# Kernel optimization log

Hardware: AMD Instinct MI355X
Metric: run time of the kernel (lower is better)

## Reference

```python
import jax, jax.numpy as jnp
import numpy as np
import math

B, H, N, D = 2, 8, 2048, 64

def setup_inputs() -> dict:
    key = jax.random.key(0)
    k1, k2, k3, k4, k5 = jax.random.split(key, 5)
    query = jax.random.normal(k1, (B, H, N, D), dtype=jnp.float32)
    k = jax.random.normal(k2, (B, H, N, D), dtype=jnp.float32)
    value = jax.random.normal(k3, (B, H, N, D), dtype=jnp.float32)
    mask = jax.random.randint(k4, (B, H, N, N), 0, 2, dtype=jnp.int32)
    p = jax.random.uniform(k5, (B, H, N, N), dtype=jnp.float32)
    return {"query": query, "key": k, "value": value, "mask": mask, "p": p}

def reference(query, key, value, mask, p):
    # scores: [B,H,N,N] = QK^T / sqrt(d)
    scores = jnp.einsum('bhqd,bhkd->bhqk', query, key) / math.sqrt(query.shape[-1])
    # additive log-probability bias
    scores = scores + jnp.log(p + 1e-12)
    # mask==0 -> -1e9
    scores = jnp.where(mask == 0, jnp.float32(-1e9), scores)
    p_attn = jax.nn.softmax(scores, axis=-1)
    out = jnp.einsum('bhqk,bhkd->bhqd', p_attn, value)
    return (out, p_attn)
```

## Files before the change

kernel.cpp:

```cpp
#include <hip/hip_runtime.h>


typedef float  f4v   __attribute__((ext_vector_type(4)));
typedef int    i4v   __attribute__((ext_vector_type(4)));
typedef __bf16 bf16x8 __attribute__((ext_vector_type(8)));
typedef unsigned short us8 __attribute__((ext_vector_type(8)));
typedef unsigned short us4 __attribute__((ext_vector_type(4)));
typedef unsigned int   u4v __attribute__((ext_vector_type(4)));

#define MFMA16(a,b,c) __builtin_amdgcn_mfma_f32_16x16x32_bf16((a),(b),(c),0,0,0)

static __device__ __forceinline__ unsigned short f2bf(float f){
  unsigned u = __builtin_bit_cast(unsigned, f);
  u += 0x7fffu + ((u >> 16) & 1u);
  return (unsigned short)(u >> 16);
}
static __device__ __forceinline__ bf16x8 ldg8(const unsigned short* p){
  u4v v = *(const u4v*)p;
  return __builtin_bit_cast(bf16x8, v);
}

__global__ void prep_qk(const float* __restrict__ Q, const float* __restrict__ K,
                        unsigned short* __restrict__ Qb, unsigned short* __restrict__ Kb){
  int i = blockIdx.x * 256 + threadIdx.x;
  int base = i * 4;
  f4v q = *(const f4v*)(Q + base);
  f4v k = *(const f4v*)(K + base);
  us4 qo, ko;
#pragma unroll
  for(int j=0;j<4;j++){ qo[j] = f2bf(q[j] * 0.125f); ko[j] = f2bf(k[j]); }
  *(us4*)(Qb + base) = qo;
  *(us4*)(Kb + base) = ko;
}

__global__ void prep_vt(const float* __restrict__ V, unsigned short* __restrict__ Vt){
  int t   = blockIdx.x * 256 + threadIdx.x;
  int bh  = t >> 14;
  int rem = t & 16383;
  int d   = rem >> 8;
  int n0  = (rem & 255) * 8;
  const float* src = V + (((long)bh*2048 + n0) * 64 + d);
  us8 o;
#pragma unroll
  for(int j=0;j<8;j++) o[j] = f2bf(src[j*64]);
  *(us8*)(Vt + ((long)(bh*64 + d)) * 2048 + n0) = o;
}

__global__ __launch_bounds__(256, 2) void attn_main(
    const float* __restrict__ P, const int* __restrict__ M,
    const unsigned short* __restrict__ Qb, const unsigned short* __restrict__ Kb,
    const unsigned short* __restrict__ Vt,
    float* __restrict__ out_o, float* __restrict__ out_p){

  __shared__ float stage[4*2*528];
  __shared__ float wred[2][4][16];
  __shared__ float obuf[4][16][64];

  const int tid  = threadIdx.x;
  const int w    = tid >> 6;
  const int lane = tid & 63;
  const int m    = lane & 15;
  const int q    = lane >> 4;
  const int bidx = blockIdx.x;
  const int bh = ((bidx & 7) << 1) | ((bidx >> 3) & 1);
  const int qt = bidx >> 4;
  const int q0 = qt << 4;
  const int wbase = w << 9;

  const long  rowQ  = (long)bh*2048 + q0 + m;
  const long  pbase = rowQ * 2048;
  const unsigned short* Qrow = Qb + rowQ * 64;
  const bf16x8 qf0 = ldg8(Qrow + q*8);
  const bf16x8 qf1 = ldg8(Qrow + 32 + q*8);
  const unsigned short* Kbh = Kb + ((long)bh << 17);
  const unsigned short* Vbh = Vt + ((long)bh << 17);

  float sreg[16][8];
  float vmax = -3.0e38f;
  float* st0 = stage + w * 1056;

#pragma unroll
  for(int c=0;c<16;c++){
    float* st = st0 + (c & 1) * 528;
    const int k0 = wbase + c*32;
    const unsigned short* Kp = Kbh + (long)(k0 + m)*64 + q*8;
    bf16x8 kf00 = ldg8(Kp);
    bf16x8 kf01 = ldg8(Kp + 32);
    bf16x8 kf10 = ldg8(Kp + 16*64);
    bf16x8 kf11 = ldg8(Kp + 16*64 + 32);
    const float* pp = P + pbase + k0 + q*8;
    f4v pv0 = *(const f4v*)pp;
    f4v pv1 = *(const f4v*)(pp + 4);
    const int* mp = M + pbase + k0 + q*8;
    i4v mv0 = *(const i4v*)mp;
    i4v mv1 = *(const i4v*)(mp + 4);

    f4v acc0 = {0.f,0.f,0.f,0.f}, acc1 = {0.f,0.f,0.f,0.f};
    acc0 = MFMA16(qf0, kf00, acc0);
    acc0 = MFMA16(qf1, kf01, acc0);
    acc1 = MFMA16(qf0, kf10, acc1);
    acc1 = MFMA16(qf1, kf11, acc1);

#pragma unroll
    for(int r=0;r<4;r++){
      st[(4*q + r)*33 + m]      = acc0[r];
      st[(4*q + r)*33 + 16 + m] = acc1[r];
    }
    float sv[8];
#pragma unroll
    for(int j=0;j<8;j++) sv[j] = st[m*33 + q*8 + j];

#pragma unroll
    for(int j=0;j<8;j++){
      float pj = (j < 4) ? pv0[j] : pv1[j-4];
      int   mj = (j < 4) ? mv0[j] : mv1[j-4];
      float s  = sv[j] + __logf(pj + 1e-12f);
      s = (mj == 0) ? -1.0e9f : s;
      sreg[c][j] = s;
      vmax = fmaxf(vmax, s);
    }
  }

  vmax = fmaxf(vmax, __shfl_xor(vmax, 16));
  vmax = fmaxf(vmax, __shfl_xor(vmax, 32));
  if(lane < 16) wred[0][w][lane] = vmax;
  __syncthreads();
  const float mrow = fmaxf(fmaxf(wred[0][0][m], wred[0][1][m]),
                           fmaxf(wred[0][2][m], wred[0][3][m]));

  float vsum = 0.f;
#pragma unroll
  for(int c=0;c<16;c++){
#pragma unroll
    for(int j=0;j<8;j++){
      float e = __expf(sreg[c][j] - mrow);
      sreg[c][j] = e;
      vsum += e;
    }
  }
  vsum += __shfl_xor(vsum, 16);
  vsum += __shfl_xor(vsum, 32);
  if(lane < 16) wred[1][w][lane] = vsum;
  __syncthreads();
  const float lsum = wred[1][0][m] + wred[1][1][m] + wred[1][2][m] + wred[1][3][m];
  const float rl = 1.0f / lsum;

  f4v o0={0.f,0.f,0.f,0.f}, o1={0.f,0.f,0.f,0.f}, o2={0.f,0.f,0.f,0.f}, o3={0.f,0.f,0.f,0.f};
#pragma unroll
  for(int c=0;c<16;c++){
    const int k0 = wbase + c*32;
    f4v w0, w1; us8 pb;
#pragma unroll
    for(int j=0;j<8;j++){
      float pr = sreg[c][j] * rl;
      if(j < 4) w0[j] = pr; else w1[j-4] = pr;
      pb[j] = f2bf(pr);
    }
    float* op = out_p + pbase + k0 + q*8;
    *(f4v*)op       = w0;
    *(f4v*)(op + 4) = w1;
    bf16x8 af = __builtin_bit_cast(bf16x8, pb);
    const unsigned short* Vp = Vbh + (long)m*2048 + k0 + q*8;
    o0 = MFMA16(af, ldg8(Vp),           o0);
    o1 = MFMA16(af, ldg8(Vp + 16*2048), o1);
    o2 = MFMA16(af, ldg8(Vp + 32*2048), o2);
    o3 = MFMA16(af, ldg8(Vp + 48*2048), o3);
  }

#pragma unroll
  for(int r=0;r<4;r++){
    obuf[w][4*q + r][m]      = o0[r];
    obuf[w][4*q + r][16 + m] = o1[r];
    obuf[w][4*q + r][32 + m] = o2[r];
    obuf[w][4*q + r][48 + m] = o3[r];
  }
  __syncthreads();
  const int row = tid >> 4, cg = (tid & 15) << 2;
  f4v a0 = *(const f4v*)&obuf[0][row][cg];
  f4v a1 = *(const f4v*)&obuf[1][row][cg];
  f4v a2 = *(const f4v*)&obuf[2][row][cg];
  f4v a3 = *(const f4v*)&obuf[3][row][cg];
  f4v s = a0 + a1 + a2 + a3;
  *(f4v*)(out_o + ((long)bh*2048 + q0 + row)*64 + cg) = s;
}

extern "C" void kernel_launch(void* const* d_in, const int* in_sizes, int n_in,
                              void* d_out, int out_size, void* d_ws, size_t ws_size,
                              hipStream_t stream){
  const float* Q = (const float*)d_in[0];
  const float* K = (const float*)d_in[1];
  const float* V = (const float*)d_in[2];
  const int*   M = (const int*)  d_in[3];
  const float* P = (const float*)d_in[4];

  float* out_o = (float*)d_out;
  float* out_p = out_o + (size_t)2*8*2048*64;

  unsigned short* Qb = (unsigned short*)d_ws;
  unsigned short* Kb = Qb + (size_t)2*8*2048*64;
  unsigned short* Vt = Kb + (size_t)2*8*2048*64;

  prep_qk<<<2048, 256, 0, stream>>>(Q, K, Qb, Kb);
  prep_vt<<<1024, 256, 0, stream>>>(V, Vt);
  attn_main<<<2048, 256, 0, stream>>>(P, M, Qb, Kb, Vt, out_o, out_p);
}
```

Baseline: 747.9 us.

## Use 8 waves per block with online softmax and fp16 score storage

The main kernel now runs 512 threads per block, so each wave covers 256 keys instead of 512. Softmax becomes an online running max and sum per chunk, and exponentials are kept in packed fp16 registers that are rescaled at write-out. The next chunk's K, P and mask loads are software-prefetched to overlap with the current chunk's compute, and the V transpose goes through an LDS tile so global accesses are coalesced. The goal is lower register pressure and more waves in flight for this memory-bound kernel, at the cost of fp16 rounding on the stored probabilities and extra exp work.

```diff
diff --git a/kernel.cpp b/kernel.cpp
--- a/kernel.cpp
+++ b/kernel.cpp
@@ -2,11 +2,13 @@
 
 
 typedef float  f4v   __attribute__((ext_vector_type(4)));
+typedef float  f2v   __attribute__((ext_vector_type(2)));
 typedef int    i4v   __attribute__((ext_vector_type(4)));
 typedef __bf16 bf16x8 __attribute__((ext_vector_type(8)));
 typedef unsigned short us8 __attribute__((ext_vector_type(8)));
 typedef unsigned short us4 __attribute__((ext_vector_type(4)));
 typedef unsigned int   u4v __attribute__((ext_vector_type(4)));
+typedef __fp16 h2v  __attribute__((ext_vector_type(2)));
 
 #define MFMA16(a,b,c) __builtin_amdgcn_mfma_f32_16x16x32_bf16((a),(b),(c),0,0,0)
 
@@ -14,6 +16,9 @@
   unsigned u = __builtin_bit_cast(unsigned, f);
   u += 0x7fffu + ((u >> 16) & 1u);
   return (unsigned short)(u >> 16);
+}
+static __device__ __forceinline__ bf16x8 bc8(u4v v){
+  return __builtin_bit_cast(bf16x8, v);
 }
 static __device__ __forceinline__ bf16x8 ldg8(const unsigned short* p){
   u4v v = *(const u4v*)p;
@@ -34,27 +39,44 @@
 }
 
 __global__ void prep_vt(const float* __restrict__ V, unsigned short* __restrict__ Vt){
-  int t   = blockIdx.x * 256 + threadIdx.x;
-  int bh  = t >> 14;
-  int rem = t & 16383;
-  int d   = rem >> 8;
-  int n0  = (rem & 255) * 8;
-  const float* src = V + (((long)bh*2048 + n0) * 64 + d);
-  us8 o;
-#pragma unroll
-  for(int j=0;j<8;j++) o[j] = f2bf(src[j*64]);
-  *(us8*)(Vt + ((long)(bh*64 + d)) * 2048 + n0) = o;
-}
-
-__global__ __launch_bounds__(256, 2) void attn_main(
-    const float* __restrict__ P, const int* __restrict__ M,
+  __shared__ float tile[64*65];
+  const int bh = blockIdx.x >> 5;
+  const int n0 = (blockIdx.x & 31) << 6;
+  const int t  = threadIdx.x;
+  {
+    const int r  = t >> 2;
+    const int c0 = (t & 3) << 4;
+    const float* src = V + ((long)bh*2048 + n0 + r)*64 + c0;
+    f4v v0 = *(const f4v*)(src);
+    f4v v1 = *(const f4v*)(src + 4);
+    f4v v2 = *(const f4v*)(src + 8);
+    f4v v3 = *(const f4v*)(src + 12);
+    float* d = tile + r*65 + c0;
+#pragma unroll
+    for(int j=0;j<4;j++){ d[j]=v0[j]; d[4+j]=v1[j]; d[8+j]=v2[j]; d[12+j]=v3[j]; }
+  }
+  __syncthreads();
+  const int d  = t >> 2;
+  const int g0 = (t & 3) << 1;
+#pragma unroll
+  for(int gi=0; gi<2; gi++){
+    const int g = g0 + gi;
+    us8 o;
+#pragma unroll
+    for(int j=0;j<8;j++) o[j] = f2bf(tile[(g*8 + j)*65 + d]);
+    *(us8*)(Vt + ((long)bh*64 + d)*2048 + n0 + g*8) = o;
+  }
+}
+
+__global__ __launch_bounds__(512, 4) void attn_main(
+    const float* __restrict__ P, const int* __restrict__ Mk,
     const unsigned short* __restrict__ Qb, const unsigned short* __restrict__ Kb,
     const unsigned short* __restrict__ Vt,
     float* __restrict__ out_o, float* __restrict__ out_p){
 
-  __shared__ float stage[4*2*528];
-  __shared__ float wred[2][4][16];
-  __shared__ float obuf[4][16][64];
+  __shared__ float smem[8*1056];
+  __shared__ float wredm[8][16];
+  __shared__ float wreds[8][16];
 
   const int tid  = threadIdx.x;
   const int w    = tid >> 6;
@@ -65,7 +87,7 @@
   const int bh = ((bidx & 7) << 1) | ((bidx >> 3) & 1);
   const int qt = bidx >> 4;
   const int q0 = qt << 4;
-  const int wbase = w << 9;
+  const int wbase = w << 8;
 
   const long  rowQ  = (long)bh*2048 + q0 + m;
   const long  pbase = rowQ * 2048;
@@ -75,86 +97,109 @@
   const unsigned short* Kbh = Kb + ((long)bh << 17);
   const unsigned short* Vbh = Vt + ((long)bh << 17);
 
-  float sreg[16][8];
-  float vmax = -3.0e38f;
-  float* st0 = stage + w * 1056;
-
-#pragma unroll
-  for(int c=0;c<16;c++){
-    float* st = st0 + (c & 1) * 528;
-    const int k0 = wbase + c*32;
-    const unsigned short* Kp = Kbh + (long)(k0 + m)*64 + q*8;
-    bf16x8 kf00 = ldg8(Kp);
-    bf16x8 kf01 = ldg8(Kp + 32);
-    bf16x8 kf10 = ldg8(Kp + 16*64);
-    bf16x8 kf11 = ldg8(Kp + 16*64 + 32);
-    const float* pp = P + pbase + k0 + q*8;
-    f4v pv0 = *(const f4v*)pp;
-    f4v pv1 = *(const f4v*)(pp + 4);
-    const int* mp = M + pbase + k0 + q*8;
-    i4v mv0 = *(const i4v*)mp;
-    i4v mv1 = *(const i4v*)(mp + 4);
-
+  const unsigned short* Kp = Kbh + (long)(wbase + m)*64 + q*8;
+  const float* pp = P  + pbase + wbase + q*8;
+  const int*   mp = Mk + pbase + wbase + q*8;
+
+  h2v   ereg[8][4];
+  float mch[8];
+  float mcur = -3.0e38f, vsum = 0.f;
+  float* st0 = smem + w*1056;
+
+  u4v k0A = *(const u4v*)(Kp);
+  u4v k1A = *(const u4v*)(Kp + 32);
+  u4v k2A = *(const u4v*)(Kp + 1024);
+  u4v k3A = *(const u4v*)(Kp + 1024 + 32);
+  f4v p0A = *(const f4v*)(pp);
+  f4v p1A = *(const f4v*)(pp + 4);
+  i4v m0A = *(const i4v*)(mp);
+  i4v m1A = *(const i4v*)(mp + 4);
+
+#pragma unroll
+  for(int c=0;c<8;c++){
+    u4v k0N,k1N,k2N,k3N; f4v p0N,p1N; i4v m0N,m1N;
+    if(c < 7){
+      const unsigned short* Kn = Kp + (c+1)*2048;
+      k0N = *(const u4v*)(Kn);
+      k1N = *(const u4v*)(Kn + 32);
+      k2N = *(const u4v*)(Kn + 1024);
+      k3N = *(const u4v*)(Kn + 1024 + 32);
+      p0N = *(const f4v*)(pp + (c+1)*32);
+      p1N = *(const f4v*)(pp + (c+1)*32 + 4);
+      m0N = *(const i4v*)(mp + (c+1)*32);
+      m1N = *(const i4v*)(mp + (c+1)*32 + 4);
+    }
     f4v acc0 = {0.f,0.f,0.f,0.f}, acc1 = {0.f,0.f,0.f,0.f};
-    acc0 = MFMA16(qf0, kf00, acc0);
-    acc0 = MFMA16(qf1, kf01, acc0);
-    acc1 = MFMA16(qf0, kf10, acc1);
-    acc1 = MFMA16(qf1, kf11, acc1);
-
+    acc0 = MFMA16(qf0, bc8(k0A), acc0);
+    acc0 = MFMA16(qf1, bc8(k1A), acc0);
+    acc1 = MFMA16(qf0, bc8(k2A), acc1);
+    acc1 = MFMA16(qf1, bc8(k3A), acc1);
+
+    float* st = st0 + (c & 1)*528;
 #pragma unroll
     for(int r=0;r<4;r++){
       st[(4*q + r)*33 + m]      = acc0[r];
       st[(4*q + r)*33 + 16 + m] = acc1[r];
     }
-    float sv[8];
-#pragma unroll
-    for(int j=0;j<8;j++) sv[j] = st[m*33 + q*8 + j];
-
+    float s[8];
 #pragma unroll
     for(int j=0;j<8;j++){
-      float pj = (j < 4) ? pv0[j] : pv1[j-4];
-      int   mj = (j < 4) ? mv0[j] : mv1[j-4];
-      float s  = sv[j] + __logf(pj + 1e-12f);
-      s = (mj == 0) ? -1.0e9f : s;
-      sreg[c][j] = s;
-      vmax = fmaxf(vmax, s);
-    }
-  }
-
-  vmax = fmaxf(vmax, __shfl_xor(vmax, 16));
-  vmax = fmaxf(vmax, __shfl_xor(vmax, 32));
-  if(lane < 16) wred[0][w][lane] = vmax;
+      float pj = (j < 4) ? p0A[j] : p1A[j-4];
+      int   mj = (j < 4) ? m0A[j] : m1A[j-4];
+      float sc = st[m*33 + q*8 + j] + __logf(pj + 1e-12f);
+      s[j] = (mj == 0) ? -1.0e9f : sc;
+    }
+    float cm = s[0];
+#pragma unroll
+    for(int j=1;j<8;j++) cm = fmaxf(cm, s[j]);
+    float mn = fmaxf(mcur, cm);
+    vsum *= __expf(mcur - mn);
+#pragma unroll
+    for(int jj=0;jj<4;jj++){
+      float e0 = __expf(s[2*jj]   - mn);
+      float e1 = __expf(s[2*jj+1] - mn);
+      vsum += e0 + e1;
+      ereg[c][jj] = __builtin_amdgcn_cvt_pkrtz(e0, e1);
+    }
+    mch[c] = mn; mcur = mn;
+
+    k0A=k0N; k1A=k1N; k2A=k2N; k3A=k3N;
+    p0A=p0N; p1A=p1N; m0A=m0N; m1A=m1N;
+  }
+
+  {
+    float om = __shfl_xor(mcur, 16), ov = __shfl_xor(vsum, 16);
+    float nm = fmaxf(mcur, om);
+    vsum = vsum*__expf(mcur - nm) + ov*__expf(om - nm); mcur = nm;
+    om = __shfl_xor(mcur, 32); ov = __shfl_xor(vsum, 32);
+    nm = fmaxf(mcur, om);
+    vsum = vsum*__expf(mcur - nm) + ov*__expf(om - nm); mcur = nm;
+  }
+  if(lane < 16){ wredm[w][lane] = mcur; wreds[w][lane] = vsum; }
   __syncthreads();
-  const float mrow = fmaxf(fmaxf(wred[0][0][m], wred[0][1][m]),
-                           fmaxf(wred[0][2][m], wred[0][3][m]));
-
-  float vsum = 0.f;
-#pragma unroll
-  for(int c=0;c<16;c++){
-#pragma unroll
-    for(int j=0;j<8;j++){
-      float e = __expf(sreg[c][j] - mrow);
-      sreg[c][j] = e;
-      vsum += e;
-    }
-  }
-  vsum += __shfl_xor(vsum, 16);
-  vsum += __shfl_xor(vsum, 32);
-  if(lane < 16) wred[1][w][lane] = vsum;
-  __syncthreads();
-  const float lsum = wred[1][0][m] + wred[1][1][m] + wred[1][2][m] + wred[1][3][m];
-  const float rl = 1.0f / lsum;
+  float Mrow = -3.0e38f;
+#pragma unroll
+  for(int p2=0;p2<8;p2++) Mrow = fmaxf(Mrow, wredm[p2][m]);
+  float l = 0.f;
+#pragma unroll
+  for(int p2=0;p2<8;p2++) l += wreds[p2][m]*__expf(wredm[p2][m] - Mrow);
+  const float rl = 1.0f / l;
 
   f4v o0={0.f,0.f,0.f,0.f}, o1={0.f,0.f,0.f,0.f}, o2={0.f,0.f,0.f,0.f}, o3={0.f,0.f,0.f,0.f};
 #pragma unroll
-  for(int c=0;c<16;c++){
+  for(int c=0;c<8;c++){
+    const float f = __expf(mch[c] - Mrow) * rl;
     const int k0 = wbase + c*32;
     f4v w0, w1; us8 pb;
 #pragma unroll
-    for(int j=0;j<8;j++){
-      float pr = sreg[c][j] * rl;
-      if(j < 4) w0[j] = pr; else w1[j-4] = pr;
-      pb[j] = f2bf(pr);
+    for(int jj=0;jj<4;jj++){
+      h2v ee = ereg[c][jj];
+      float pr0 = (float)ee[0] * f;
+      float pr1 = (float)ee[1] * f;
+      if(jj < 2){ w0[2*jj] = pr0; w0[2*jj+1] = pr1; }
+      else      { w1[2*jj-4] = pr0; w1[2*jj-3] = pr1; }
+      pb[2*jj]   = f2bf(pr0);
+      pb[2*jj+1] = f2bf(pr1);
     }
     float* op = out_p + pbase + k0 + q*8;
     *(f4v*)op       = w0;
@@ -167,21 +212,24 @@
     o3 = MFMA16(af, ldg8(Vp + 48*2048), o3);
   }
 
+  float* ob = smem + w*1056;
 #pragma unroll
   for(int r=0;r<4;r++){
-    obuf[w][4*q + r][m]      = o0[r];
-    obuf[w][4*q + r][16 + m] = o1[r];
-    obuf[w][4*q + r][32 + m] = o2[r];
-    obuf[w][4*q + r][48 + m] = o3[r];
+    ob[(4*q + r)*66 + m]      = o0[r];
+    ob[(4*q + r)*66 + 16 + m] = o1[r];
+    ob[(4*q + r)*66 + 32 + m] = o2[r];
+    ob[(4*q + r)*66 + 48 + m] = o3[r];
   }
   __syncthreads();
-  const int row = tid >> 4, cg = (tid & 15) << 2;
-  f4v a0 = *(const f4v*)&obuf[0][row][cg];
-  f4v a1 = *(const f4v*)&obuf[1][row][cg];
-  f4v a2 = *(const f4v*)&obuf[2][row][cg];
-  f4v a3 = *(const f4v*)&obuf[3][row][cg];
-  f4v s = a0 + a1 + a2 + a3;
-  *(f4v*)(out_o + ((long)bh*2048 + q0 + row)*64 + cg) = s;
+  const int row = tid >> 5;
+  const int c2  = (tid & 31) << 1;
+  f2v s2 = {0.f, 0.f};
+#pragma unroll
+  for(int p2=0;p2<8;p2++){
+    f2v a = *(const f2v*)(smem + p2*1056 + row*66 + c2);
+    s2 += a;
+  }
+  *(f2v*)(out_o + ((long)bh*2048 + q0 + row)*64 + c2) = s2;
 }
 
 extern "C" void kernel_launch(void* const* d_in, const int* in_sizes, int n_in,
@@ -201,6 +249,6 @@
   unsigned short* Vt = Kb + (size_t)2*8*2048*64;
 
   prep_qk<<<2048, 256, 0, stream>>>(Q, K, Qb, Kb);
-  prep_vt<<<1024, 256, 0, stream>>>(V, Vt);
-  attn_main<<<2048, 256, 0, stream>>>(P, M, Qb, Kb, Vt, out_o, out_p);
-}
+  prep_vt<<<512, 256, 0, stream>>>(V, Vt);
+  attn_main<<<2048, 512, 0, stream>>>(P, M, Qb, Kb, Vt, out_o, out_p);
+}
```

Result: no change. 749.0 us (+0.2%).
